# Kernel optimization log

Hardware: AMD Instinct MI355X
Metric: run time of the kernel (lower is better)

The kernel has to match this reference:

```python
import jax, jax.numpy as jnp
import numpy as np

NUM_HEADS = 8
EPS = 1e-12  # torch F.normalize eps


def _conv1x1(x, W, b):
    # x: [B,C,H,W], W: [O,C], b: [O]
    return jnp.einsum('bchw,oc->bohw', x, W) + b[None, :, None, None]


def _mdta(x, wq, bq, wk, bk, wv, bv, temp):
    # Restormer-style channel attention (dropout = identity in eval).
    B, C, H, W = x.shape
    hd = C // NUM_HEADS

    def proj(Wm, bm):
        return _conv1x1(x, Wm, bm).reshape(B, NUM_HEADS, hd, H * W)

    q = proj(wq, bq)
    k = proj(wk, bk)
    v = proj(wv, bv)
    qn = q / jnp.maximum(jnp.linalg.norm(q, axis=-1, keepdims=True), EPS)
    kn = k / jnp.maximum(jnp.linalg.norm(k, axis=-1, keepdims=True), EPS)
    attn = jnp.einsum('bhcn,bhdn->bhcd', qn, kn) * temp  # temp: [heads,1,1]
    attn = jax.nn.softmax(attn, axis=-1)
    out = jnp.einsum('bhcd,bhdn->bhcn', attn, v) + v
    return out.reshape(B, C, H, W) + x


def setup_inputs() -> dict:
    key = jax.random.key(0)
    ks = jax.random.split(key, 10)
    B, C, H, W = 4, 64, 256, 256
    s = 1.0 / np.sqrt(C)
    f32 = jnp.float32
    return {
        'x': jax.random.normal(ks[0], (B, C, H, W), f32),
        'y': jax.random.normal(ks[1], (B, C, H, W), f32),
        'wq': jax.random.normal(ks[2], (C, C), f32) * s,
        'bq': jnp.zeros((C,), f32),
        'wk': jax.random.normal(ks[3], (C, C), f32) * s,
        'bk': jnp.zeros((C,), f32),
        'wv': jax.random.normal(ks[4], (C, C), f32) * s,
        'bv': jnp.zeros((C,), f32),
        'temp': jnp.ones((NUM_HEADS, 1, 1), f32),
        'w_ch': jax.random.normal(ks[5], (C, C), f32) * s,
        'b_ch': jnp.zeros((C,), f32),
        'w_y': jax.random.normal(ks[6], (C, C), f32) * s,
        'w_aw': jax.random.normal(ks[7], (1, C), f32) * s,
        'b_aw': jnp.zeros((1,), f32),
    }


def reference(x, y, wq, bq, wk, bk, wv, bv, temp, w_ch, b_ch, w_y, w_aw, b_aw):
    B, C, H, W = x.shape
    x_attn = _mdta(x, wq, bq, wk, bk, wv, bv, temp)
    y_attn = _mdta(y, wq, bq, wk, bk, wv, bv, temp)
    x_t = x_attn.transpose(0, 2, 3, 1)  # [B,H,W,C]
    y_t = y_attn.transpose(0, 2, 3, 1)
    # spatial gating: tanh(affine(x) + affine(y)) -> scalar logit per pixel
    xk = jnp.tanh(jnp.einsum('bhwc,oc->bhwo', x_t, w_ch) + b_ch
                  + jnp.einsum('bhwc,oc->bhwo', y_t, w_y))
    logits = (jnp.einsum('bhwo,ko->bhwk', xk, w_aw) + b_aw)[..., 0]  # [B,H,W]
    weight = jax.nn.softmax(logits.reshape(B, -1), axis=-1).reshape(B, 1, H, W)
    # result = x_1 * weight + x_1 (x_1 is the ORIGINAL input, permuted)
    result1 = x * (weight + 1.0)
    result2 = y * (weight + 1.0)
    return result1, result2
```

## Files before the change

kernel.cpp:

```cpp
#include <hip/hip_runtime.h>
#include <hip/hip_bf16.h>

typedef unsigned short ushortt;

#define BB 4
#define CC 64
#define NN 65536
#define HEADS 8

typedef __attribute__((ext_vector_type(8))) short bf16x8;
typedef __attribute__((ext_vector_type(4))) float f32x4;
typedef __attribute__((ext_vector_type(4))) unsigned int u32x4;

#define OFF_PG   0UL
#define OFF_G    1343488UL
#define OFF_S    1376256UL
#define OFF_U    1376768UL
#define OFF_V    1409536UL
#define OFF_PS   1442304UL
#define OFF_CV2  1443328UL
#define OFF_P    1475072UL
#define OFF_L    1508096UL

__device__ __forceinline__ ushortt f2bf(float f) {
    union { float f; unsigned int i; } v; v.f = f;
    unsigned int x = v.i;
    unsigned int r = x + 0x7FFFu + ((x >> 16) & 1u);
    return (ushortt)(r >> 16);
}

__device__ __forceinline__ bf16x8 ld_cvt(const float* p) {
    const f32x4 a = *(const f32x4*)p;
    const f32x4 b = *(const f32x4*)(p + 4);
    bf16x8 r;
    r[0] = (short)f2bf(a[0]); r[1] = (short)f2bf(a[1]);
    r[2] = (short)f2bf(a[2]); r[3] = (short)f2bf(a[3]);
    r[4] = (short)f2bf(b[0]); r[5] = (short)f2bf(b[1]);
    r[6] = (short)f2bf(b[2]); r[7] = (short)f2bf(b[3]);
    return r;
}

#define PSEL 0x07060302u
__device__ __forceinline__ bf16x8 pack_trunc(const f32x4 a, const f32x4 b) {
    union { f32x4 f; u32x4 u; } ua, ub;
    ua.f = a; ub.f = b;
    union { u32x4 u; bf16x8 s; } out;
    out.u[0] = __builtin_amdgcn_perm(ua.u[1], ua.u[0], PSEL);
    out.u[1] = __builtin_amdgcn_perm(ua.u[3], ua.u[2], PSEL);
    out.u[2] = __builtin_amdgcn_perm(ub.u[1], ub.u[0], PSEL);
    out.u[3] = __builtin_amdgcn_perm(ub.u[3], ub.u[2], PSEL);
    return out.s;
}
__device__ __forceinline__ bf16x8 ld_trunc(const float* p) {
    return pack_trunc(*(const f32x4*)p, *(const f32x4*)(p + 4));
}

__device__ __forceinline__ float fast_tanh(float t) {
    const float e = __expf(t + t);
    return 1.f - 2.f * __builtin_amdgcn_rcpf(e + 1.f);
}

#define MFMA(a,b,c) __builtin_amdgcn_mfma_f32_16x16x32_bf16(a,b,c,0,0,0)

__global__ __launch_bounds__(256) void k_gram(const float* __restrict__ x,
                                              const float* __restrict__ y,
                                              float* __restrict__ ws) {
    const int chunk = blockIdx.x;
    const int b = blockIdx.y, z = blockIdx.z;
    const float* X = (z ? y : x) + (size_t)b * CC * NN;
    const int tid = threadIdx.x;
    const int wid = tid >> 6, lane = tid & 63;
    const int lr = lane & 15, lk = lane >> 4;

    f32x4 accG[10];
    f32x4 accS[4];
#pragma unroll
    for (int t = 0; t < 10; ++t) accG[t] = (f32x4){0.f, 0.f, 0.f, 0.f};
#pragma unroll
    for (int g = 0; g < 4; ++g) accS[g] = (f32x4){0.f, 0.f, 0.f, 0.f};
    bf16x8 ones;
#pragma unroll
    for (int j = 0; j < 8; ++j) ones[j] = (short)0x3F80;

    const int p0 = chunk * 1024 + wid * 256;
    for (int ks = 0; ks < 8; ++ks) {
        const int pc = p0 + ks * 32 + lk * 8;
        bf16x8 a0 = ld_trunc(X + (size_t)(0 * 16 + lr) * NN + pc);
        bf16x8 a1 = ld_trunc(X + (size_t)(1 * 16 + lr) * NN + pc);
        bf16x8 a2 = ld_trunc(X + (size_t)(2 * 16 + lr) * NN + pc);
        bf16x8 a3 = ld_trunc(X + (size_t)(3 * 16 + lr) * NN + pc);
        accG[0] = MFMA(a0, a0, accG[0]);
        accG[1] = MFMA(a0, a1, accG[1]);
        accG[2] = MFMA(a0, a2, accG[2]);
        accG[3] = MFMA(a0, a3, accG[3]);
        accG[4] = MFMA(a1, a1, accG[4]);
        accG[5] = MFMA(a1, a2, accG[5]);
        accG[6] = MFMA(a1, a3, accG[6]);
        accG[7] = MFMA(a2, a2, accG[7]);
        accG[8] = MFMA(a2, a3, accG[8]);
        accG[9] = MFMA(a3, a3, accG[9]);
        accS[0] = MFMA(a0, ones, accS[0]);
        accS[1] = MFMA(a1, ones, accS[1]);
        accS[2] = MFMA(a2, ones, accS[2]);
        accS[3] = MFMA(a3, ones, accS[3]);
    }

    __shared__ float red[2624];
    for (int i = tid; i < 2624; i += 256) red[i] = 0.f;
    __syncthreads();
    for (int w = 0; w < 4; ++w) {
        if (wid == w) {
#pragma unroll
            for (int ti = 0; ti < 4; ++ti)
#pragma unroll
                for (int tj = ti; tj < 4; ++tj) {
                    const int t = ti * 4 - ti * (ti + 1) / 2 + tj;
#pragma unroll
                    for (int r = 0; r < 4; ++r)
                        red[t * 256 + (lk * 4 + r) * 16 + lr] += accG[t][r];
                }
            if (lr == 0) {
#pragma unroll
                for (int g = 0; g < 4; ++g)
#pragma unroll
                    for (int r = 0; r < 4; ++r)
                        red[2560 + g * 16 + lk * 4 + r] += accS[g][r];
            }
        }
        __syncthreads();
    }
    const int slot = (z * 4 + b) * 64 + chunk;
    float* outp = ws + OFF_PG + (size_t)slot * 2624;
    for (int i = tid; i < 2624; i += 256) outp[i] = red[i];
}

__global__ void k_reduce(float* __restrict__ ws) {
    const int gid = blockIdx.x * 256 + threadIdx.x;
    if (gid < 8 * 4096) {
        const int zb = gid >> 12;
        const int e = gid & 4095;
        const int row = e >> 6, col = e & 63;
        const int ti = row >> 4, tj = col >> 4;
        int t, elem;
        if (ti <= tj) { t = ti * 4 - ti * (ti + 1) / 2 + tj; elem = (row & 15) * 16 + (col & 15); }
        else          { t = tj * 4 - tj * (tj + 1) / 2 + ti; elem = (col & 15) * 16 + (row & 15); }
        const float* base = ws + OFF_PG + (size_t)(zb * 64) * 2624 + t * 256 + elem;
        float s = 0.f;
        for (int c = 0; c < 64; ++c) s += base[(size_t)c * 2624];
        ws[OFF_G + gid] = s;
    } else if (gid < 8 * 4096 + 8 * 64) {
        const int g2 = gid - 8 * 4096;
        const int zb = g2 >> 6, e = g2 & 63;
        const float* base = ws + OFF_PG + (size_t)(zb * 64) * 2624 + 2560 + e;
        float s = 0.f;
        for (int c = 0; c < 64; ++c) s += base[(size_t)c * 2624];
        ws[OFF_S + g2] = s;
    }
}

__global__ void k_uv(const float* __restrict__ wq, const float* __restrict__ wk,
                     float* __restrict__ ws) {
    const int gid = blockIdx.x * 256 + threadIdx.x;
    const int which = gid >> 15;
    const int rem = gid & 32767;
    const int zb = rem >> 12;
    const int e = rem & 4095;
    const int r = e >> 6, j = e & 63;
    const float* W = which ? wk : wq;
    const float* Gm = ws + OFF_G + (size_t)zb * 4096;
    float acc = 0.f;
    for (int i = 0; i < 64; ++i) acc += W[r * 64 + i] * Gm[i * 64 + j];
    ws[(which ? OFF_V : OFF_U) + (size_t)zb * 4096 + e] = acc;
}

__global__ __launch_bounds__(256) void k_attn2(
        const float* __restrict__ wq, const float* __restrict__ bq,
        const float* __restrict__ wk, const float* __restrict__ bk,
        const float* __restrict__ wv, const float* __restrict__ bv,
        const float* __restrict__ temp,
        const float* __restrict__ w_ch, const float* __restrict__ b_ch,
        const float* __restrict__ w_y, float* __restrict__ ws) {
    const int zb = blockIdx.x;
    const int z = zb >> 2;
    const int tid = threadIdx.x;

    __shared__ float Ul[4096], Vl[4096];
    __shared__ float wql[4096], wkl[4096], wvl[4096], wsl[4096];
    __shared__ float sl[64], dq[64], dk[64], wqs[64], wks[64];
    __shared__ float qkl[512], Al[512], cstz[64];
    __shared__ float ph1s[64][4][4];

    {
        const float* Ug = ws + OFF_U + (size_t)zb * 4096;
        const float* Vg = ws + OFF_V + (size_t)zb * 4096;
        const float* wsel = z ? w_y : w_ch;
        for (int i = tid * 4; i < 4096; i += 1024) {
            *(f32x4*)(Ul + i)  = *(const f32x4*)(Ug + i);
            *(f32x4*)(Vl + i)  = *(const f32x4*)(Vg + i);
            *(f32x4*)(wql + i) = *(const f32x4*)(wq + i);
            *(f32x4*)(wkl + i) = *(const f32x4*)(wk + i);
            *(f32x4*)(wvl + i) = *(const f32x4*)(wv + i);
            *(f32x4*)(wsl + i) = *(const f32x4*)(wsel + i);
        }
        if (tid < 64) sl[tid] = ws[OFF_S + (size_t)zb * 64 + tid];
    }
    __syncthreads();

    {
        const int r = tid >> 2, q = tid & 3;
        float swq = 0.f, swk = 0.f, sqq = 0.f, skk = 0.f;
#pragma unroll
        for (int jj = 0; jj < 16; ++jj) {
            const int j = q * 16 + jj;
            const float svj = sl[j];
            const float wqv = wql[r * 64 + j];
            const float wkv = wkl[r * 64 + j];
            swq += wqv * svj; swk += wkv * svj;
            sqq += Ul[r * 64 + j] * wqv;
            skk += Vl[r * 64 + j] * wkv;
        }
        ph1s[r][q][0] = swq; ph1s[r][q][1] = swk;
        ph1s[r][q][2] = sqq; ph1s[r][q][3] = skk;
    }
    __syncthreads();
    if (tid < 64) {
        const int r = tid;
        const float swq = ph1s[r][0][0] + ph1s[r][1][0] + ph1s[r][2][0] + ph1s[r][3][0];
        const float swk = ph1s[r][0][1] + ph1s[r][1][1] + ph1s[r][2][1] + ph1s[r][3][1];
        float sqq = ph1s[r][0][2] + ph1s[r][1][2] + ph1s[r][2][2] + ph1s[r][3][2];
        float skk = ph1s[r][0][3] + ph1s[r][1][3] + ph1s[r][2][3] + ph1s[r][3][3];
        const float bqv = bq[r], bkv = bk[r];
        sqq += 2.f * bqv * swq + 65536.f * bqv * bqv;
        skk += 2.f * bkv * swk + 65536.f * bkv * bkv;
        dq[r] = fmaxf(sqrtf(fmaxf(sqq, 0.f)), 1e-12f);
        dk[r] = fmaxf(sqrtf(fmaxf(skk, 0.f)), 1e-12f);
        wqs[r] = swq; wks[r] = swk;
    }
    __syncthreads();
    for (int kq = 0; kq < 2; ++kq) {
        const int id = tid + kq * 256;
        const int h = id >> 6, o = (id >> 3) & 7, p = id & 7;
        const int r = h * 8 + o, c = h * 8 + p;
        float acc = 0.f;
#pragma unroll 8
        for (int j = 0; j < 64; ++j) acc += Ul[r * 64 + j] * wkl[c * 64 + j];
        const float bqv = bq[r], bkv = bk[c];
        acc += bqv * wks[c] + bkv * wqs[r] + 65536.f * bqv * bkv;
        qkl[id] = acc;
    }
    __syncthreads();
    if (tid < 64) {
        const int r = tid, h = r >> 3;
        const float tv = temp[h];
        float L[8];
        float m = -1e30f;
#pragma unroll
        for (int p = 0; p < 8; ++p) {
            const float v = qkl[h * 64 + (r & 7) * 8 + p] / (dq[r] * dk[h * 8 + p]) * tv;
            L[p] = v; m = fmaxf(m, v);
        }
        float s = 0.f;
#pragma unroll
        for (int p = 0; p < 8; ++p) { L[p] = __expf(L[p] - m); s += L[p]; }
        const float inv = 1.f / s;
        float cz = bv[r];
#pragma unroll
        for (int p = 0; p < 8; ++p) {
            const float a = L[p] * inv;
            Al[r * 8 + p] = a;
            cz += a * bv[h * 8 + p];
        }
        cstz[r] = cz;
    }
    __syncthreads();
    for (int o4 = tid; o4 < 4096; o4 += 256) {
        const int o = o4 >> 6, j = o4 & 63, hj = j >> 3;
        float m = 0.f;
#pragma unroll
        for (int p = 0; p < 8; ++p)
            m += wsl[o * 64 + hj * 8 + p] * Al[(hj * 8 + p) * 8 + (j & 7)];
        Vl[o4] = wsl[o4] + m;
    }
    __syncthreads();
    for (int o4 = tid; o4 < 4096; o4 += 256) {
        const int o = o4 >> 6, c = o4 & 63;
        float acc = wsl[o4];
#pragma unroll 8
        for (int j = 0; j < 64; ++j) acc += Vl[o * 64 + j] * wvl[j * 64 + c];
        ws[OFF_P + (size_t)zb * 4096 + o4] = acc;
    }
    if (tid < 64) {
        const int o = tid;
        float acc = z ? 0.f : b_ch[o];
        for (int r = 0; r < 64; ++r) acc += wsl[o * 64 + r] * cstz[r];
        ws[OFF_CV2 + (size_t)zb * 64 + o] = acc;
    }
}

__global__ __launch_bounds__(256, 2) void k_logits(const float* __restrict__ x,
        const float* __restrict__ y, const float* __restrict__ w_aw,
        const float* __restrict__ b_aw, float* __restrict__ ws) {
    const int b = blockIdx.y;
    const int bx = blockIdx.x;
    const int tid = threadIdx.x;
    const int wid = tid >> 6, lane = tid & 63;
    const int lr = lane & 15, lg = lane >> 4;

    __shared__ float XT[64 * 65], YT[64 * 65];
    __shared__ float wsum[4];

    const float* Pbase = ws + OFF_P + (size_t)b * 4096;
    const float* Qbase = ws + OFF_P + (size_t)(4 + b) * 4096;

    bf16x8 AP[4][2], AQ[4][2];
#pragma unroll
    for (int ot = 0; ot < 4; ++ot)
#pragma unroll
        for (int ks = 0; ks < 2; ++ks) {
            const int off = (ot * 16 + lr) * 64 + ks * 32 + lg * 8;
            AP[ot][ks] = ld_cvt(Pbase + off);
            AQ[ot][ks] = ld_cvt(Qbase + off);
        }

    float awr[4][4], cvr[4][4];
#pragma unroll
    for (int ot = 0; ot < 4; ++ot)
#pragma unroll
        for (int r = 0; r < 4; ++r) {
            const int o = ot * 16 + lg * 4 + r;
            awr[ot][r] = w_aw[o];
            cvr[ot][r] = ws[OFF_CV2 + b * 64 + o] + ws[OFF_CV2 + (4 + b) * 64 + o];
        }
    const float baw0 = b_aw[0];

    const float* xb = x + (size_t)b * CC * NN;
    const float* yb = y + (size_t)b * CC * NN;
    const int srow = tid >> 2;
    const int scol = (tid & 3) * 16;

    float esum = 0.f;
#pragma unroll 1
    for (int ch = 0; ch < 8; ++ch) {
        const int p0 = bx * 512 + ch * 64;
        {
            const float* xs = xb + (size_t)srow * NN + p0 + scol;
            const float* ys = yb + (size_t)srow * NN + p0 + scol;
            const f32x4 x0 = *(const f32x4*)xs;
            const f32x4 x1 = *(const f32x4*)(xs + 4);
            const f32x4 x2 = *(const f32x4*)(xs + 8);
            const f32x4 x3 = *(const f32x4*)(xs + 12);
            const f32x4 y0 = *(const f32x4*)ys;
            const f32x4 y1 = *(const f32x4*)(ys + 4);
            const f32x4 y2 = *(const f32x4*)(ys + 8);
            const f32x4 y3 = *(const f32x4*)(ys + 12);
            float* xd = XT + srow * 65 + scol;
            float* yd = YT + srow * 65 + scol;
#pragma unroll
            for (int i = 0; i < 4; ++i) {
                xd[i] = x0[i]; xd[4 + i] = x1[i]; xd[8 + i] = x2[i]; xd[12 + i] = x3[i];
                yd[i] = y0[i]; yd[4 + i] = y1[i]; yd[8 + i] = y2[i]; yd[12 + i] = y3[i];
            }
        }
        __syncthreads();
        const int pl = wid * 16 + lr;
        const unsigned int* XU = (const unsigned int*)XT;
        const unsigned int* YU = (const unsigned int*)YT;
        bf16x8 BX[2], BY[2];
#pragma unroll
        for (int ks = 0; ks < 2; ++ks) {
            const int c0 = ks * 32 + lg * 8;
            union { u32x4 u; bf16x8 s; } fx, fy;
#pragma unroll
            for (int q = 0; q < 4; ++q) {
                const unsigned int xa = XU[(c0 + 2 * q) * 65 + pl];
                const unsigned int xbv = XU[(c0 + 2 * q + 1) * 65 + pl];
                fx.u[q] = __builtin_amdgcn_perm(xbv, xa, PSEL);
                const unsigned int ya = YU[(c0 + 2 * q) * 65 + pl];
                const unsigned int ybv = YU[(c0 + 2 * q + 1) * 65 + pl];
                fy.u[q] = __builtin_amdgcn_perm(ybv, ya, PSEL);
            }
            BX[ks] = fx.s; BY[ks] = fy.s;
        }
        f32x4 Cf[4];
#pragma unroll
        for (int ot = 0; ot < 4; ++ot) Cf[ot] = (f32x4){0.f, 0.f, 0.f, 0.f};
#pragma unroll
        for (int ot = 0; ot < 4; ++ot)
#pragma unroll
            for (int ks = 0; ks < 2; ++ks) {
                Cf[ot] = MFMA(AP[ot][ks], BX[ks], Cf[ot]);
                Cf[ot] = MFMA(AQ[ot][ks], BY[ks], Cf[ot]);
            }
        float partial = 0.f;
#pragma unroll
        for (int ot = 0; ot < 4; ++ot)
#pragma unroll
            for (int r = 0; r < 4; ++r)
                partial += awr[ot][r] * fast_tanh(Cf[ot][r] + cvr[ot][r]);
        partial += __shfl_xor(partial, 16);
        partial += __shfl_xor(partial, 32);
        const float e = __expf(partial + baw0);
        if (lane < 16)
            ws[OFF_L + (size_t)b * NN + p0 + wid * 16 + lane] = e;
        esum += e * 0.25f;
        __syncthreads();
    }
#pragma unroll
    for (int d = 1; d < 64; d <<= 1) esum += __shfl_xor(esum, d);
    if (lane == 0) wsum[wid] = esum;
    __syncthreads();
    if (tid == 0)
        ws[OFF_PS + (size_t)b * 128 + bx] = wsum[0] + wsum[1] + wsum[2] + wsum[3];
}

__global__ __launch_bounds__(256) void k_final(const float* __restrict__ x,
        const float* __restrict__ y, const float* __restrict__ ws,
        float* __restrict__ out) {
    const int gid = blockIdx.x * 256 + threadIdx.x;
    const int b = gid >> 19;
    const int lane = threadIdx.x & 63;
    const float* ps = ws + OFF_PS + (size_t)b * 128;
    float s = ps[lane] + ps[64 + lane];
#pragma unroll
    for (int d = 1; d < 64; d <<= 1) s += __shfl_xor(s, d);
    const float inv = 1.f / s;

    const int rem = gid & 524287;
    const int c = rem >> 13;
    const int n0 = (rem & 8191) * 8;
    const float* w = ws + OFF_L + (size_t)b * NN + n0;
    const f32x4 w0 = *(const f32x4*)w;
    const f32x4 w1 = *(const f32x4*)(w + 4);
    const size_t idx = ((size_t)(b * 64 + c)) * NN + n0;
    const f32x4 x0 = *(const f32x4*)(x + idx);
    const f32x4 x1 = *(const f32x4*)(x + idx + 4);
    const f32x4 y0 = *(const f32x4*)(y + idx);
    const f32x4 y1 = *(const f32x4*)(y + idx + 4);
    f32x4 o0, o1, o2, o3;
#pragma unroll
    for (int j = 0; j < 4; ++j) {
        const float s0 = 1.f + w0[j] * inv;
        const float s1 = 1.f + w1[j] * inv;
        o0[j] = x0[j] * s0;
        o1[j] = x1[j] * s1;
        o2[j] = y0[j] * s0;
        o3[j] = y1[j] * s1;
    }
    *(f32x4*)(out + idx) = o0;
    *(f32x4*)(out + idx + 4) = o1;
    *(f32x4*)(out + 16777216UL + idx) = o2;
    *(f32x4*)(out + 16777216UL + idx + 4) = o3;
}

extern "C" void kernel_launch(void* const* d_in, const int* in_sizes, int n_in,
                              void* d_out, int out_size, void* d_ws, size_t ws_size,
                              hipStream_t stream) {
    const float* x    = (const float*)d_in[0];
    const float* y    = (const float*)d_in[1];
    const float* wq   = (const float*)d_in[2];
    const float* bq   = (const float*)d_in[3];
    const float* wk   = (const float*)d_in[4];
    const float* bk   = (const float*)d_in[5];
    const float* wv   = (const float*)d_in[6];
    const float* bv   = (const float*)d_in[7];
    const float* temp = (const float*)d_in[8];
    const float* wch  = (const float*)d_in[9];
    const float* bch  = (const float*)d_in[10];
    const float* wyy  = (const float*)d_in[11];
    const float* waw  = (const float*)d_in[12];
    const float* baw  = (const float*)d_in[13];
    float* out = (float*)d_out;
    float* ws = (float*)d_ws;

    hipLaunchKernelGGL(k_gram, dim3(64, 4, 2), dim3(256), 0, stream, x, y, ws);
    hipLaunchKernelGGL(k_reduce, dim3(130), dim3(256), 0, stream, ws);
    hipLaunchKernelGGL(k_uv, dim3(256), dim3(256), 0, stream, wq, wk, ws);
    hipLaunchKernelGGL(k_attn2, dim3(8), dim3(256), 0, stream,
                       wq, bq, wk, bk, wv, bv, temp, wch, bch, wyy, ws);
    hipLaunchKernelGGL(k_logits, dim3(128, 4), dim3(256), 0, stream, x, y, waw, baw, ws);
    hipLaunchKernelGGL(k_final, dim3(8192), dim3(256), 0, stream, x, y, ws, out);
}
```

Baseline: 129.6 us.

## Double-buffer the x/y LDS tiles in k_logits with register prefetch

In k_logits, the global loads of the next 64-pixel x/y chunk are now issued into registers before the current chunk's MFMA and tanh work. They are written into a second LDS buffer afterwards, so one barrier per iteration replaces two. The aim is to hide global-memory latency behind compute. The cost is doubled LDS per block (about 66 KB) and extra live registers, which could limit the two-blocks-per-CU occupancy target.

Measured after the change: 128.8 us. No clear change (-0.6%).

```diff
diff --git a/kernel.cpp b/kernel.cpp
--- a/kernel.cpp
+++ b/kernel.cpp
@@ -306,7 +306,7 @@
     const int wid = tid >> 6, lane = tid & 63;
     const int lr = lane & 15, lg = lane >> 4;
 
-    __shared__ float XT[64 * 65], YT[64 * 65];
+    __shared__ float XT[2][64 * 65], YT[2][64 * 65];
     __shared__ float wsum[4];
 
     const float* Pbase = ws + OFF_P + (size_t)b * 4096;
@@ -337,34 +337,43 @@
     const float* yb = y + (size_t)b * CC * NN;
     const int srow = tid >> 2;
     const int scol = (tid & 3) * 16;
+    const size_t sbase = (size_t)srow * NN + bx * 512 + scol;
+    const int ldso = srow * 65 + scol;
+
+    f32x4 rx0, rx1, rx2, rx3, ry0, ry1, ry2, ry3;
+    {
+        const float* xs = xb + sbase;
+        const float* ys = yb + sbase;
+        rx0 = *(const f32x4*)xs;       rx1 = *(const f32x4*)(xs + 4);
+        rx2 = *(const f32x4*)(xs + 8); rx3 = *(const f32x4*)(xs + 12);
+        ry0 = *(const f32x4*)ys;       ry1 = *(const f32x4*)(ys + 4);
+        ry2 = *(const f32x4*)(ys + 8); ry3 = *(const f32x4*)(ys + 12);
+        float* xd = &XT[0][ldso];
+        float* yd = &YT[0][ldso];
+#pragma unroll
+        for (int i = 0; i < 4; ++i) {
+            xd[i] = rx0[i]; xd[4 + i] = rx1[i]; xd[8 + i] = rx2[i]; xd[12 + i] = rx3[i];
+            yd[i] = ry0[i]; yd[4 + i] = ry1[i]; yd[8 + i] = ry2[i]; yd[12 + i] = ry3[i];
+        }
+    }
+    __syncthreads();
 
     float esum = 0.f;
 #pragma unroll 1
     for (int ch = 0; ch < 8; ++ch) {
+        const int cur = ch & 1;
+        if (ch < 7) {
+            const float* xs = xb + sbase + (ch + 1) * 64;
+            const float* ys = yb + sbase + (ch + 1) * 64;
+            rx0 = *(const f32x4*)xs;       rx1 = *(const f32x4*)(xs + 4);
+            rx2 = *(const f32x4*)(xs + 8); rx3 = *(const f32x4*)(xs + 12);
+            ry0 = *(const f32x4*)ys;       ry1 = *(const f32x4*)(ys + 4);
+            ry2 = *(const f32x4*)(ys + 8); ry3 = *(const f32x4*)(ys + 12);
+        }
         const int p0 = bx * 512 + ch * 64;
-        {
-            const float* xs = xb + (size_t)srow * NN + p0 + scol;
-            const float* ys = yb + (size_t)srow * NN + p0 + scol;
-            const f32x4 x0 = *(const f32x4*)xs;
-            const f32x4 x1 = *(const f32x4*)(xs + 4);
-            const f32x4 x2 = *(const f32x4*)(xs + 8);
-            const f32x4 x3 = *(const f32x4*)(xs + 12);
-            const f32x4 y0 = *(const f32x4*)ys;
-            const f32x4 y1 = *(const f32x4*)(ys + 4);
-            const f32x4 y2 = *(const f32x4*)(ys + 8);
-            const f32x4 y3 = *(const f32x4*)(ys + 12);
-            float* xd = XT + srow * 65 + scol;
-            float* yd = YT + srow * 65 + scol;
-#pragma unroll
-            for (int i = 0; i < 4; ++i) {
-                xd[i] = x0[i]; xd[4 + i] = x1[i]; xd[8 + i] = x2[i]; xd[12 + i] = x3[i];
-                yd[i] = y0[i]; yd[4 + i] = y1[i]; yd[8 + i] = y2[i]; yd[12 + i] = y3[i];
-            }
-        }
-        __syncthreads();
         const int pl = wid * 16 + lr;
-        const unsigned int* XU = (const unsigned int*)XT;
-        const unsigned int* YU = (const unsigned int*)YT;
+        const unsigned int* XU = (const unsigned int*)XT[cur];
+        const unsigned int* YU = (const unsigned int*)YT[cur];
         bf16x8 BX[2], BY[2];
 #pragma unroll
         for (int ks = 0; ks < 2; ++ks) {
@@ -403,6 +412,15 @@
         if (lane < 16)
             ws[OFF_L + (size_t)b * NN + p0 + wid * 16 + lane] = e;
         esum += e * 0.25f;
+        if (ch < 7) {
+            float* xd = &XT[cur ^ 1][ldso];
+            float* yd = &YT[cur ^ 1][ldso];
+#pragma unroll
+            for (int i = 0; i < 4; ++i) {
+                xd[i] = rx0[i]; xd[4 + i] = rx1[i]; xd[8 + i] = rx2[i]; xd[12 + i] = rx3[i];
+                yd[i] = ry0[i]; yd[4 + i] = ry1[i]; yd[8 + i] = ry2[i]; yd[12 + i] = ry3[i];
+            }
+        }
         __syncthreads();
     }
 #pragma unroll
```
